# Performance work log

Hardware: AMD Instinct MI355X
Metric: run time of the kernel (lower is better)

## Reference

```python
import jax, jax.numpy as jnp
import numpy as np

E, FF, H, PE = 256, 1024, 8, 32

def _ln(x, g, b, eps=1e-5):
    m = jnp.mean(x, axis=-1, keepdims=True)
    v = jnp.var(x, axis=-1, keepdims=True)
    return (x - m) / jnp.sqrt(v + eps) * g + b

def setup_inputs() -> dict:
    key = jax.random.key(0)
    ks = jax.random.split(key, 24)
    B, N, NH = 2, 8192, 8
    w = lambda i, shape: (jax.random.normal(ks[i], shape, jnp.float32) * 0.02)
    return {
        'x': jax.random.normal(ks[0], (B, N, NH, E), jnp.float32),
        'pos1': jax.random.normal(ks[1], (B, N, NH, 2), jnp.float32),
        'pos2': jax.random.normal(ks[2], (B, N, NH, 2), jnp.float32),
        'W_in': w(3, (E, E)), 'g_in': jnp.ones((E,), jnp.float32), 'b_in': jnp.zeros((E,), jnp.float32),
        'Wq': w(4, (E, E)), 'bq': jnp.zeros((E,), jnp.float32),
        'Wk': w(5, (E, E)), 'bk': jnp.zeros((E,), jnp.float32),
        'Wv': w(6, (E, E)), 'bv': jnp.zeros((E,), jnp.float32),
        'Wo': w(7, (E, E)), 'bo': jnp.zeros((E,), jnp.float32),
        'W_pos': w(8, (4, PE)), 'W_bias': w(9, (PE, H)),
        'W_ff1': w(10, (E, FF)), 'W_ff2': w(11, (FF, E)),
        'g1': jnp.ones((E,), jnp.float32), 'b1': jnp.zeros((E,), jnp.float32),
        'g2': jnp.ones((E,), jnp.float32), 'b2': jnp.zeros((E,), jnp.float32),
    }

def reference(x, pos1, pos2, W_in, g_in, b_in, Wq, bq, Wk, bk, Wv, bv, Wo, bo,
              W_pos, W_bias, W_ff1, W_ff2, g1, b1, g2, b2):
    B, N, NH, e = x.shape
    d = e // H
    # input_mlp: Linear(no bias) + LayerNorm
    t = _ln(x @ W_in, g_in, b_in).reshape(B * N, NH, e)  # (BN, nh, E); q=k=v=t
    q = (t @ Wq + bq).reshape(B * N, NH, H, d)
    k = (t @ Wk + bk).reshape(B * N, NH, H, d)
    v = (t @ Wv + bv).reshape(B * N, NH, H, d)
    scores = jnp.einsum('bqhd,bkhd->bhqk', q, k) / jnp.sqrt(jnp.float32(d))  # (BN,H,nh,nh)
    # positional bias: pos_embedder(pos1,pos2) -> emb_proj_bias -> per-key per-head bias
    emb = jax.nn.silu(jnp.concatenate([pos1, pos2], axis=-1) @ W_pos)  # (B,N,nh,PE)
    bias = (emb @ W_bias).reshape(B * N, NH, H)  # (BN, nh_key, H)
    scores = scores + jnp.transpose(bias, (0, 2, 1))[:, :, None, :]  # broadcast over queries
    att = jax.nn.softmax(scores, axis=-1)
    att_out = jnp.einsum('bhqk,bkhd->bqhd', att, v).reshape(B * N, NH, e)
    att_out = att_out @ Wo + bo
    h1 = _ln(t + att_out, g1, b1)  # q_res residual on pre-projection q
    h2 = _ln(h1 + jax.nn.silu(h1 @ W_ff1) @ W_ff2, g2, b2)
    return h2.reshape(B, N, NH, e)
```

## Files before the change

### kernel.cpp

```cpp
#include <hip/hip_runtime.h>
#include <cstdint>
#include <cstddef>

typedef unsigned short ushort_t;
typedef __attribute__((ext_vector_type(8))) short short8;
typedef __attribute__((ext_vector_type(4))) short short4v;
typedef __attribute__((ext_vector_type(4))) float floatx4;

__device__ __forceinline__ float b2f(ushort_t u) {
    unsigned v = ((unsigned)u) << 16;
    return __builtin_bit_cast(float, v);
}
__device__ __forceinline__ float b2fs(short s) { return b2f((ushort_t)s); }
__device__ __forceinline__ ushort_t f2b(float f) {
    unsigned u = __builtin_bit_cast(unsigned, f);
    u += 0x7fffu + ((u >> 16) & 1u);
    return (ushort_t)(u >> 16);
}

__device__ __forceinline__ void load_lds16(const ushort_t* g, ushort_t* l) {
    __builtin_amdgcn_global_load_lds(
        (const __attribute__((address_space(1))) void*)g,
        (__attribute__((address_space(3))) void*)l, 16, 0, 0);
}

template <int NT, bool A_F32, bool HAS_BIAS, bool DO_SILU>
__global__ __launch_bounds__(256, 2) void gemm_areg(
    const void* __restrict__ Ap, const ushort_t* __restrict__ BT,
    const float* __restrict__ bias, ushort_t* __restrict__ out)
{
    constexpr int K = 256;
    constexpr int ldN = NT * 128;
    __shared__ __align__(16) ushort_t Bs[128 * 256];

    const int tid = threadIdx.x;
    const int w = tid >> 6, lane = tid & 63;
    const int wm = w >> 1, wn = w & 1;
    const int quad = lane >> 4, r = lane & 15;
    const size_t m0 = (size_t)blockIdx.x * 128;

    short8 af[4][8];
    if (A_F32) {
        const float* A = (const float*)Ap;
#pragma unroll
        for (int mt = 0; mt < 4; ++mt) {
            const float* rp = A + (m0 + wm * 64 + mt * 16 + r) * K + quad * 8;
#pragma unroll
            for (int kk = 0; kk < 8; ++kk) {
                float4 a = *(const float4*)(rp + kk * 32);
                float4 b = *(const float4*)(rp + kk * 32 + 4);
                short8 o;
                o[0] = (short)f2b(a.x); o[1] = (short)f2b(a.y);
                o[2] = (short)f2b(a.z); o[3] = (short)f2b(a.w);
                o[4] = (short)f2b(b.x); o[5] = (short)f2b(b.y);
                o[6] = (short)f2b(b.z); o[7] = (short)f2b(b.w);
                af[mt][kk] = o;
            }
        }
    } else {
        const ushort_t* A = (const ushort_t*)Ap;
#pragma unroll
        for (int mt = 0; mt < 4; ++mt) {
            const ushort_t* rp = A + (m0 + wm * 64 + mt * 16 + r) * K + quad * 8;
#pragma unroll
            for (int kk = 0; kk < 8; ++kk)
                af[mt][kk] = *(const short8*)(rp + kk * 32);
        }
    }

    const int srow_off = w * 2 + (lane >> 5);
    const int sslot = (lane & 31) ^ (srow_off & 7);
    const int rsw = (r & 7) << 3;

    for (int nt_i = 0; nt_i < NT; ++nt_i) {
        const int n0 = nt_i * 128;
        __syncthreads();
#pragma unroll
        for (int i = 0; i < 16; ++i) {
            int row = i * 8 + srow_off;
            load_lds16(BT + (size_t)(n0 + row) * K + sslot * 8,
                       Bs + (i * 8 + w * 2) * 256);
        }
        __syncthreads();

        floatx4 acc[4][4];
#pragma unroll
        for (int nt = 0; nt < 4; ++nt)
#pragma unroll
            for (int mt = 0; mt < 4; ++mt)
#pragma unroll
                for (int rg = 0; rg < 4; ++rg) acc[nt][mt][rg] = 0.f;

#pragma unroll
        for (int kk = 0; kk < 8; ++kk) {
            const int koff = (kk * 32 + quad * 8) ^ rsw;
#pragma unroll
            for (int nt = 0; nt < 4; ++nt) {
                int col = wn * 64 + nt * 16 + r;
                short8 bf_ = *(const short8*)(Bs + col * 256 + koff);
#pragma unroll
                for (int mt = 0; mt < 4; ++mt)
                    acc[nt][mt] = __builtin_amdgcn_mfma_f32_16x16x32_bf16(
                        af[mt][kk], bf_, acc[nt][mt], 0, 0, 0);
            }
        }
#pragma unroll
        for (int nt = 0; nt < 4; ++nt) {
            int col = n0 + wn * 64 + nt * 16 + r;
            float bv = 0.f;
            if (HAS_BIAS) bv = bias[col];
#pragma unroll
            for (int mt = 0; mt < 4; ++mt) {
#pragma unroll
                for (int rg = 0; rg < 4; ++rg) {
                    size_t row = m0 + wm * 64 + mt * 16 + quad * 4 + rg;
                    float v = acc[nt][mt][rg] + bv;
                    if (DO_SILU) v = v / (1.f + __expf(-v));
                    out[row * ldN + col] = f2b(v);
                }
            }
        }
    }
}

__global__ __launch_bounds__(256, 2) void gemm_wide(
    const ushort_t* __restrict__ A, const ushort_t* __restrict__ BT,
    ushort_t* __restrict__ out)
{
    constexpr int K = 1024, N = 256;
    __shared__ __align__(16) ushort_t As[128 * 64];
    __shared__ __align__(16) ushort_t Bs[256 * 64];

    const int tid = threadIdx.x;
    const int w = tid >> 6, lane = tid & 63;
    const int wm = w >> 1, wn = w & 1;
    const int quad = lane >> 4, r = lane & 15;
    const size_t m0 = (size_t)blockIdx.x * 128;

    const int sslot8 = (lane & 7) ^ ((lane >> 3) & 7);
    const int rsw = (r & 7) << 3;

    floatx4 acc[8][4];
#pragma unroll
    for (int nt = 0; nt < 8; ++nt)
#pragma unroll
        for (int mt = 0; mt < 4; ++mt)
#pragma unroll
            for (int rg = 0; rg < 4; ++rg) acc[nt][mt][rg] = 0.f;

    for (int kc = 0; kc < K / 64; ++kc) {
        __syncthreads();
#pragma unroll
        for (int i = 0; i < 4; ++i) {
            int row = i * 32 + w * 8 + (lane >> 3);
            load_lds16(A + (m0 + row) * K + kc * 64 + sslot8 * 8,
                       As + (i * 32 + w * 8) * 64);
        }
#pragma unroll
        for (int i = 0; i < 8; ++i) {
            int row = i * 32 + w * 8 + (lane >> 3);
            load_lds16(BT + (size_t)row * K + kc * 64 + sslot8 * 8,
                       Bs + (i * 32 + w * 8) * 64);
        }
        __syncthreads();
#pragma unroll
        for (int ks = 0; ks < 2; ++ks) {
            const int koff = (ks * 32 + quad * 8) ^ rsw;
            short8 af[4];
#pragma unroll
            for (int mt = 0; mt < 4; ++mt)
                af[mt] = *(const short8*)(As + (wm * 64 + mt * 16 + r) * 64 + koff);
#pragma unroll
            for (int nt = 0; nt < 8; ++nt) {
                short8 bf_ = *(const short8*)(Bs + (wn * 128 + nt * 16 + r) * 64 + koff);
#pragma unroll
                for (int mt = 0; mt < 4; ++mt)
                    acc[nt][mt] = __builtin_amdgcn_mfma_f32_16x16x32_bf16(
                        af[mt], bf_, acc[nt][mt], 0, 0, 0);
            }
        }
    }
#pragma unroll
    for (int nt = 0; nt < 8; ++nt) {
        int col = wn * 128 + nt * 16 + r;
#pragma unroll
        for (int mt = 0; mt < 4; ++mt)
#pragma unroll
            for (int rg = 0; rg < 4; ++rg) {
                size_t row = m0 + wm * 64 + mt * 16 + quad * 4 + rg;
                out[row * N + col] = f2b(acc[nt][mt][rg]);
            }
    }
}

template <bool OUT_F32>
__global__ __launch_bounds__(256) void ln_kernel(
    const ushort_t* __restrict__ y, const ushort_t* __restrict__ res,
    const float* __restrict__ g, const float* __restrict__ b,
    void* __restrict__ outv)
{
    const int w = threadIdx.x >> 6;
    const int lane = threadIdx.x & 63;
    const size_t row = (size_t)blockIdx.x * 4 + w;
    const size_t base = row * 256 + lane * 4;

    short4v vy = *(const short4v*)(y + base);
    float v[4];
#pragma unroll
    for (int j = 0; j < 4; ++j) v[j] = b2fs(vy[j]);
    if (res) {
        short4v vr = *(const short4v*)(res + base);
#pragma unroll
        for (int j = 0; j < 4; ++j) v[j] += b2fs(vr[j]);
    }
    float s = v[0] + v[1] + v[2] + v[3];
    float sq = v[0] * v[0] + v[1] * v[1] + v[2] * v[2] + v[3] * v[3];
#pragma unroll
    for (int off = 32; off > 0; off >>= 1) {
        s += __shfl_xor(s, off, 64);
        sq += __shfl_xor(sq, off, 64);
    }
    float mean = s * (1.f / 256.f);
    float var = sq * (1.f / 256.f) - mean * mean;
    float rstd = rsqrtf(var + 1e-5f);
    if (OUT_F32) {
        float4 ov;
        int col = lane * 4;
        ov.x = (v[0] - mean) * rstd * g[col + 0] + b[col + 0];
        ov.y = (v[1] - mean) * rstd * g[col + 1] + b[col + 1];
        ov.z = (v[2] - mean) * rstd * g[col + 2] + b[col + 2];
        ov.w = (v[3] - mean) * rstd * g[col + 3] + b[col + 3];
        *(float4*)((float*)outv + base) = ov;
    } else {
        short4v ov;
#pragma unroll
        for (int j = 0; j < 4; ++j) {
            int col = lane * 4 + j;
            float o = (v[j] - mean) * rstd * g[col] + b[col];
            ov[j] = (short)f2b(o);
        }
        *(short4v*)((ushort_t*)outv + base) = ov;
    }
}

__global__ __launch_bounds__(256) void attn_kernel(
    const ushort_t* __restrict__ qkv,
    const float* __restrict__ pos1, const float* __restrict__ pos2,
    const float* __restrict__ Wpos, const float* __restrict__ Wbias,
    ushort_t* __restrict__ att_out)
{
    __shared__ __align__(16) ushort_t qkv_s[4][8 * 768];
    __shared__ float bias_s[4][8][8];
    __shared__ float wpos_s[128];
    __shared__ float wbias_s[256];

    const int tid = threadIdx.x;
    if (tid < 128) wpos_s[tid] = Wpos[tid];
    wbias_s[tid] = Wbias[tid];

    const int w = tid >> 6;
    const int lane = tid & 63;
    const int tok = blockIdx.x * 4 + w;

    const ushort_t* src = qkv + (size_t)tok * 8 * 768;
    for (int c = lane; c < 768; c += 64)
        *(short8*)(qkv_s[w] + c * 8) = *(const short8*)(src + c * 8);
    __syncthreads();

    {
        const int j = lane >> 3, h = lane & 7;
        const size_t pbase = ((size_t)tok * 8 + j) * 2;
        float p0 = pos1[pbase], p1 = pos1[pbase + 1];
        float p2 = pos2[pbase], p3 = pos2[pbase + 1];
        float acc = 0.f;
#pragma unroll
        for (int p = 0; p < 32; ++p) {
            float e = p0 * wpos_s[p] + p1 * wpos_s[32 + p] + p2 * wpos_s[64 + p] + p3 * wpos_s[96 + p];
            e = e / (1.f + __expf(-e));
            acc += e * wbias_s[p * 8 + h];
        }
        bias_s[w][j][h] = acc;
    }
    __syncthreads();

    const int i = lane >> 3, h = lane & 7;
    const ushort_t* qrow = qkv_s[w] + i * 768 + h * 32;
    float q[32];
#pragma unroll
    for (int c = 0; c < 4; ++c) {
        short8 t8 = *(const short8*)(qrow + c * 8);
#pragma unroll
        for (int e = 0; e < 8; ++e) q[c * 8 + e] = b2fs(t8[e]);
    }
    float s[8];
#pragma unroll
    for (int jj = 0; jj < 8; ++jj) {
        const ushort_t* krow = qkv_s[w] + jj * 768 + 256 + h * 32;
        float d = 0.f;
#pragma unroll
        for (int c = 0; c < 4; ++c) {
            short8 t8 = *(const short8*)(krow + c * 8);
#pragma unroll
            for (int e = 0; e < 8; ++e) d += q[c * 8 + e] * b2fs(t8[e]);
        }
        s[jj] = d * 0.17677669529663688f + bias_s[w][jj][h];
    }
    float mx = s[0];
#pragma unroll
    for (int jj = 1; jj < 8; ++jj) mx = fmaxf(mx, s[jj]);
    float l = 0.f;
#pragma unroll
    for (int jj = 0; jj < 8; ++jj) { s[jj] = __expf(s[jj] - mx); l += s[jj]; }
    float rl = 1.f / l;
    float o[32];
#pragma unroll
    for (int e = 0; e < 32; ++e) o[e] = 0.f;
#pragma unroll
    for (int jj = 0; jj < 8; ++jj) {
        float p = s[jj] * rl;
        const ushort_t* vrow = qkv_s[w] + jj * 768 + 512 + h * 32;
#pragma unroll
        for (int c = 0; c < 4; ++c) {
            short8 t8 = *(const short8*)(vrow + c * 8);
#pragma unroll
            for (int e = 0; e < 8; ++e) o[c * 8 + e] += p * b2fs(t8[e]);
        }
    }
    ushort_t* orow = att_out + ((size_t)tok * 8 + i) * 256 + h * 32;
#pragma unroll
    for (int c = 0; c < 4; ++c) {
        short8 t8;
#pragma unroll
        for (int e = 0; e < 8; ++e) t8[e] = (short)f2b(o[c * 8 + e]);
        *(short8*)(orow + c * 8) = t8;
    }
}

__global__ void transpose_kernel(const float* __restrict__ in,
                                 ushort_t* __restrict__ out, int K, int N)
{
    int idx = blockIdx.x * 256 + threadIdx.x;
    if (idx < K * N) {
        int k = idx / N, n = idx % N;
        out[n * K + k] = f2b(in[idx]);
    }
}

__global__ void pack_bias_kernel(const float* a, const float* b,
                                 const float* c, float* out)
{
    int t = blockIdx.x * 256 + threadIdx.x;
    if (t < 256) out[t] = a[t];
    else if (t < 512) out[t] = b[t - 256];
    else if (t < 768) out[t] = c[t - 512];
}

extern "C" void kernel_launch(void* const* d_in, const int* in_sizes, int n_in,
                              void* d_out, int out_size, void* d_ws, size_t ws_size,
                              hipStream_t stream)
{
    const float* x     = (const float*)d_in[0];
    const float* pos1  = (const float*)d_in[1];
    const float* pos2  = (const float*)d_in[2];
    const float* W_in  = (const float*)d_in[3];
    const float* g_in  = (const float*)d_in[4];
    const float* b_in  = (const float*)d_in[5];
    const float* Wq    = (const float*)d_in[6];
    const float* bq    = (const float*)d_in[7];
    const float* Wk    = (const float*)d_in[8];
    const float* bk    = (const float*)d_in[9];
    const float* Wv    = (const float*)d_in[10];
    const float* bv    = (const float*)d_in[11];
    const float* Wo    = (const float*)d_in[12];
    const float* bo    = (const float*)d_in[13];
    const float* W_pos = (const float*)d_in[14];
    const float* W_bias= (const float*)d_in[15];
    const float* W_ff1 = (const float*)d_in[16];
    const float* W_ff2 = (const float*)d_in[17];
    const float* g1    = (const float*)d_in[18];
    const float* b1    = (const float*)d_in[19];
    const float* g2    = (const float*)d_in[20];
    const float* b2    = (const float*)d_in[21];

    const int M = in_sizes[0] / 256;
    const int ntok = M / 8;

    ushort_t* ws    = (ushort_t*)d_ws;
    ushort_t* WinT  = ws;
    ushort_t* WqkvT = ws + 65536;
    ushort_t* WoT   = ws + 262144;
    ushort_t* Wff1T = ws + 327680;
    ushort_t* Wff2T = ws + 589824;
    float*    bqkv  = (float*)(ws + 851968);
    ushort_t* bufA  = (ushort_t*)((char*)d_ws + (2ull << 20));
    ushort_t* bufB  = bufA + (size_t)M * 256;
    ushort_t* bufC  = bufB + (size_t)M * 256;

    transpose_kernel<<<256, 256, 0, stream>>>(W_in, WinT, 256, 256);
    transpose_kernel<<<256, 256, 0, stream>>>(Wq, WqkvT, 256, 256);
    transpose_kernel<<<256, 256, 0, stream>>>(Wk, WqkvT + 65536, 256, 256);
    transpose_kernel<<<256, 256, 0, stream>>>(Wv, WqkvT + 131072, 256, 256);
    transpose_kernel<<<256, 256, 0, stream>>>(Wo, WoT, 256, 256);
    transpose_kernel<<<1024, 256, 0, stream>>>(W_ff1, Wff1T, 256, 1024);
    transpose_kernel<<<1024, 256, 0, stream>>>(W_ff2, Wff2T, 1024, 256);
    pack_bias_kernel<<<3, 256, 0, stream>>>(bq, bk, bv, bqkv);

    dim3 blk(256);
    gemm_areg<2, true, false, false><<<M / 128, blk, 0, stream>>>(x, WinT, nullptr, bufA);
    ln_kernel<false><<<M / 4, blk, 0, stream>>>(bufA, nullptr, g_in, b_in, bufB);
    gemm_areg<6, false, true, false><<<M / 128, blk, 0, stream>>>(bufB, WqkvT, bqkv, bufC);
    attn_kernel<<<ntok / 4, blk, 0, stream>>>(bufC, pos1, pos2, W_pos, W_bias, bufA);
    gemm_areg<2, false, true, false><<<M / 128, blk, 0, stream>>>(bufA, WoT, bo, bufC);
    ln_kernel<false><<<M / 4, blk, 0, stream>>>(bufC, bufB, g1, b1, bufA);
    gemm_areg<8, false, false, true><<<M / 128, blk, 0, stream>>>(bufA, Wff1T, nullptr, bufC);
    gemm_wide<<<M / 128, blk, 0, stream>>>(bufC, Wff2T, bufB);
    ln_kernel<true><<<M / 4, blk, 0, stream>>>(bufB, bufA, g2, b2, d_out);
}
```

Baseline: 914.6 us.

## Double-buffer B tiles in GEMMs and transpose MFMA operands for vector stores

Both GEMM kernels now use double-buffered LDS and prefetch the next B (and A) chunk with async global-to-LDS loads while MFMAs run on the current buffer. Explicit vmcnt waits and barriers replace the paired __syncthreads. Swapping the MFMA operand order transposes the accumulator layout, so each lane writes four consecutive output columns as one 8-byte store instead of four scalar stores. Per-block LDS and the chunk sizes change, and the hand-tuned vmcnt counts must match the number of outstanding loads to stay correct.

```diff
diff --git a/kernel.cpp b/kernel.cpp
--- a/kernel.cpp
+++ b/kernel.cpp
@@ -31,13 +31,31 @@
 {
     constexpr int K = 256;
     constexpr int ldN = NT * 128;
-    __shared__ __align__(16) ushort_t Bs[128 * 256];
+    constexpr int NH = NT * 2;
+    __shared__ __align__(16) ushort_t Bs[2][64 * 256];
 
     const int tid = threadIdx.x;
     const int w = tid >> 6, lane = tid & 63;
     const int wm = w >> 1, wn = w & 1;
     const int quad = lane >> 4, r = lane & 15;
     const size_t m0 = (size_t)blockIdx.x * 128;
+
+    const int srow_off = w * 2 + (lane >> 5);
+    const int sslot = (lane & 31) ^ srow_off;
+    const int rsw = (r & 7) << 3;
+
+#define STAGE_H(h)                                                        \
+    {                                                                     \
+        const int h_ = (h);                                               \
+        _Pragma("unroll")                                                 \
+        for (int i_ = 0; i_ < 8; ++i_) {                                  \
+            int row_ = i_ * 8 + srow_off;                                 \
+            load_lds16(BT + (size_t)(h_ * 64 + row_) * K + sslot * 8,     \
+                       &Bs[h_ & 1][(i_ * 8 + w * 2) * 256]);              \
+        }                                                                 \
+    }
+
+    STAGE_H(0);
 
     short8 af[4][8];
     if (A_F32) {
@@ -68,24 +86,15 @@
         }
     }
 
-    const int srow_off = w * 2 + (lane >> 5);
-    const int sslot = (lane & 31) ^ (srow_off & 7);
-    const int rsw = (r & 7) << 3;
-
-    for (int nt_i = 0; nt_i < NT; ++nt_i) {
-        const int n0 = nt_i * 128;
-        __syncthreads();
-#pragma unroll
-        for (int i = 0; i < 16; ++i) {
-            int row = i * 8 + srow_off;
-            load_lds16(BT + (size_t)(n0 + row) * K + sslot * 8,
-                       Bs + (i * 8 + w * 2) * 256);
-        }
-        __syncthreads();
-
-        floatx4 acc[4][4];
-#pragma unroll
-        for (int nt = 0; nt < 4; ++nt)
+    asm volatile("s_waitcnt vmcnt(0)" ::: "memory");
+    __builtin_amdgcn_s_barrier();
+
+    for (int p = 0; p < NH; ++p) {
+        if (p + 1 < NH) STAGE_H(p + 1);
+
+        floatx4 acc[2][4];
+#pragma unroll
+        for (int nt = 0; nt < 2; ++nt)
 #pragma unroll
             for (int mt = 0; mt < 4; ++mt)
 #pragma unroll
@@ -95,32 +104,40 @@
         for (int kk = 0; kk < 8; ++kk) {
             const int koff = (kk * 32 + quad * 8) ^ rsw;
 #pragma unroll
-            for (int nt = 0; nt < 4; ++nt) {
-                int col = wn * 64 + nt * 16 + r;
-                short8 bf_ = *(const short8*)(Bs + col * 256 + koff);
+            for (int nt = 0; nt < 2; ++nt) {
+                int cl = wn * 32 + nt * 16 + r;
+                short8 bf_ = *(const short8*)(&Bs[p & 1][cl * 256 + koff]);
 #pragma unroll
                 for (int mt = 0; mt < 4; ++mt)
                     acc[nt][mt] = __builtin_amdgcn_mfma_f32_16x16x32_bf16(
-                        af[mt][kk], bf_, acc[nt][mt], 0, 0, 0);
+                        bf_, af[mt][kk], acc[nt][mt], 0, 0, 0);
             }
         }
 #pragma unroll
-        for (int nt = 0; nt < 4; ++nt) {
-            int col = n0 + wn * 64 + nt * 16 + r;
-            float bv = 0.f;
-            if (HAS_BIAS) bv = bias[col];
+        for (int nt = 0; nt < 2; ++nt) {
+            const int colb = p * 64 + wn * 32 + nt * 16 + quad * 4;
+            float b4[4] = {0.f, 0.f, 0.f, 0.f};
+            if (HAS_BIAS) {
+                float4 bb = *(const float4*)(bias + colb);
+                b4[0] = bb.x; b4[1] = bb.y; b4[2] = bb.z; b4[3] = bb.w;
+            }
 #pragma unroll
             for (int mt = 0; mt < 4; ++mt) {
+                size_t row = m0 + wm * 64 + mt * 16 + r;
+                short4v ov;
 #pragma unroll
                 for (int rg = 0; rg < 4; ++rg) {
-                    size_t row = m0 + wm * 64 + mt * 16 + quad * 4 + rg;
-                    float v = acc[nt][mt][rg] + bv;
+                    float v = acc[nt][mt][rg] + b4[rg];
                     if (DO_SILU) v = v / (1.f + __expf(-v));
-                    out[row * ldN + col] = f2b(v);
+                    ov[rg] = (short)f2b(v);
                 }
+                *(short4v*)(out + row * ldN + colb) = ov;
             }
         }
-    }
+        asm volatile("s_waitcnt vmcnt(8)" ::: "memory");
+        __builtin_amdgcn_s_barrier();
+    }
+#undef STAGE_H
 }
 
 __global__ __launch_bounds__(256, 2) void gemm_wide(
@@ -128,8 +145,8 @@
     ushort_t* __restrict__ out)
 {
     constexpr int K = 1024, N = 256;
-    __shared__ __align__(16) ushort_t As[128 * 64];
-    __shared__ __align__(16) ushort_t Bs[256 * 64];
+    __shared__ __align__(16) ushort_t As[2][128 * 32];
+    __shared__ __align__(16) ushort_t Bs[2][256 * 32];
 
     const int tid = threadIdx.x;
     const int w = tid >> 6, lane = tid & 63;
@@ -137,8 +154,25 @@
     const int quad = lane >> 4, r = lane & 15;
     const size_t m0 = (size_t)blockIdx.x * 128;
 
-    const int sslot8 = (lane & 7) ^ ((lane >> 3) & 7);
-    const int rsw = (r & 7) << 3;
+    const int srow = lane >> 2;
+    const int sslot = (lane & 3) ^ (srow & 3);
+
+#define STAGE_C(c)                                                        \
+    {                                                                     \
+        const int c_ = (c);                                               \
+        _Pragma("unroll")                                                 \
+        for (int i_ = 0; i_ < 2; ++i_) {                                  \
+            int rb_ = (w * 2 + i_) * 16;                                  \
+            load_lds16(A + (m0 + rb_ + srow) * K + c_ * 32 + sslot * 8,   \
+                       &As[c_ & 1][rb_ * 32]);                            \
+        }                                                                 \
+        _Pragma("unroll")                                                 \
+        for (int i_ = 0; i_ < 4; ++i_) {                                  \
+            int rb_ = (w * 4 + i_) * 16;                                  \
+            load_lds16(BT + (size_t)(rb_ + srow) * K + c_ * 32 + sslot * 8,\
+                       &Bs[c_ & 1][rb_ * 32]);                            \
+        }                                                                 \
+    }
 
     floatx4 acc[8][4];
 #pragma unroll
@@ -148,48 +182,43 @@
 #pragma unroll
             for (int rg = 0; rg < 4; ++rg) acc[nt][mt][rg] = 0.f;
 
-    for (int kc = 0; kc < K / 64; ++kc) {
-        __syncthreads();
-#pragma unroll
-        for (int i = 0; i < 4; ++i) {
-            int row = i * 32 + w * 8 + (lane >> 3);
-            load_lds16(A + (m0 + row) * K + kc * 64 + sslot8 * 8,
-                       As + (i * 32 + w * 8) * 64);
-        }
-#pragma unroll
-        for (int i = 0; i < 8; ++i) {
-            int row = i * 32 + w * 8 + (lane >> 3);
-            load_lds16(BT + (size_t)row * K + kc * 64 + sslot8 * 8,
-                       Bs + (i * 32 + w * 8) * 64);
-        }
-        __syncthreads();
-#pragma unroll
-        for (int ks = 0; ks < 2; ++ks) {
-            const int koff = (ks * 32 + quad * 8) ^ rsw;
-            short8 af[4];
+    STAGE_C(0);
+    asm volatile("s_waitcnt vmcnt(0)" ::: "memory");
+    __builtin_amdgcn_s_barrier();
+
+    const int ko = (quad ^ (r & 3)) * 8;
+
+    for (int c = 0; c < K / 32; ++c) {
+        if (c + 1 < K / 32) STAGE_C(c + 1);
+
+        short8 af_[4];
+#pragma unroll
+        for (int mt = 0; mt < 4; ++mt)
+            af_[mt] = *(const short8*)(&As[c & 1][(wm * 64 + mt * 16 + r) * 32 + ko]);
+#pragma unroll
+        for (int nt = 0; nt < 8; ++nt) {
+            short8 bf_ = *(const short8*)(&Bs[c & 1][(wn * 128 + nt * 16 + r) * 32 + ko]);
 #pragma unroll
             for (int mt = 0; mt < 4; ++mt)
-                af[mt] = *(const short8*)(As + (wm * 64 + mt * 16 + r) * 64 + koff);
-#pragma unroll
-            for (int nt = 0; nt < 8; ++nt) {
-                short8 bf_ = *(const short8*)(Bs + (wn * 128 + nt * 16 + r) * 64 + koff);
-#pragma unroll
-                for (int mt = 0; mt < 4; ++mt)
-                    acc[nt][mt] = __builtin_amdgcn_mfma_f32_16x16x32_bf16(
-                        af[mt], bf_, acc[nt][mt], 0, 0, 0);
-            }
-        }
-    }
+                acc[nt][mt] = __builtin_amdgcn_mfma_f32_16x16x32_bf16(
+                    bf_, af_[mt], acc[nt][mt], 0, 0, 0);
+        }
+        asm volatile("s_waitcnt vmcnt(0)" ::: "memory");
+        __builtin_amdgcn_s_barrier();
+    }
+#undef STAGE_C
+
 #pragma unroll
     for (int nt = 0; nt < 8; ++nt) {
-        int col = wn * 128 + nt * 16 + r;
-#pragma unroll
-        for (int mt = 0; mt < 4; ++mt)
-#pragma unroll
-            for (int rg = 0; rg < 4; ++rg) {
-                size_t row = m0 + wm * 64 + mt * 16 + quad * 4 + rg;
-                out[row * N + col] = f2b(acc[nt][mt][rg]);
-            }
+        const int colb = wn * 128 + nt * 16 + quad * 4;
+#pragma unroll
+        for (int mt = 0; mt < 4; ++mt) {
+            size_t row = m0 + wm * 64 + mt * 16 + r;
+            short4v ov;
+#pragma unroll
+            for (int rg = 0; rg < 4; ++rg) ov[rg] = (short)f2b(acc[nt][mt][rg]);
+            *(short4v*)(out + row * N + colb) = ov;
+        }
     }
 }
 
```

Result: no change. 926.8 us (+1.3%).
